# Kernel tuning notes

Hardware: AMD Instinct MI355X
Metric: run time of the kernel (lower is better)

The kernel has to match this reference:

```python
import jax, jax.numpy as jnp
import numpy as np

DEPTH = 4
NUM_INTERNAL = 2 ** DEPTH - 1  # 15
NUM_LEAVES = 2 ** DEPTH        # 16
INPUT_DIM = 1024
NUM_CLASSES = 100
LEAF_HIDDEN = 256
BATCH = 4096
TAU = 1.0
EPS = 1e-10


def setup_inputs() -> dict:
    key = jax.random.key(0)
    ks = jax.random.split(key, 8)
    x = jax.random.normal(ks[0], (BATCH, INPUT_DIM), dtype=jnp.float32)
    gumbel_u = jax.random.uniform(ks[1], (NUM_INTERNAL, BATCH, INPUT_DIM), dtype=jnp.float32)
    feature_logits = jax.random.normal(ks[2], (NUM_INTERNAL, INPUT_DIM), dtype=jnp.float32) * 0.1
    split_thresholds = jnp.zeros((NUM_INTERNAL,), dtype=jnp.float32)
    feature_weights = jax.random.normal(ks[3], (NUM_INTERNAL, INPUT_DIM), dtype=jnp.float32) / np.sqrt(INPUT_DIM)
    # leaf MLPs, kaiming-normal init (fan_in), zero bias
    W1 = jax.random.normal(ks[4], (NUM_LEAVES, LEAF_HIDDEN, INPUT_DIM), dtype=jnp.float32) * np.sqrt(2.0 / INPUT_DIM)
    b1 = jnp.zeros((NUM_LEAVES, LEAF_HIDDEN), dtype=jnp.float32)
    W2 = jax.random.normal(ks[5], (NUM_LEAVES, NUM_CLASSES, LEAF_HIDDEN), dtype=jnp.float32) * np.sqrt(2.0 / LEAF_HIDDEN)
    b2 = jnp.zeros((NUM_LEAVES, NUM_CLASSES), dtype=jnp.float32)
    return {
        'x': x, 'gumbel_u': gumbel_u,
        'feature_logits': feature_logits, 'split_thresholds': split_thresholds,
        'feature_weights': feature_weights, 'W1': W1, 'b1': b1, 'W2': W2, 'b2': b2,
    }


def reference(x, gumbel_u, feature_logits, split_thresholds, feature_weights, W1, b1, W2, b2):
    # --- Gumbel-softmax feature gating (soft, tau=TAU) for ALL nodes at once ---
    g = -jnp.log(-jnp.log(gumbel_u + EPS) + EPS)                 # [N, B, D]
    imp = jax.nn.softmax((feature_logits[:, None, :] + g) / TAU, axis=-1)  # [N, B, D]
    # aggregated split value: sum_d x * importance * feature_weight
    agg = jnp.einsum('bd,nbd,nd->nb', x, imp, feature_weights)   # [N, B]
    split_prob = jax.nn.sigmoid((agg - split_thresholds[:, None]) / TAU)   # [N, B]

    # --- leaf routing probabilities (level-order traversal) ---
    probs = jnp.ones((1, x.shape[0]), dtype=x.dtype)             # [1, B]
    for level in range(DEPTH):
        n = 2 ** level
        s = jax.lax.dynamic_slice_in_dim(split_prob, n - 1, n, axis=0)  # [n, B]
        # order per node: left then right -> interleave
        probs = jnp.stack([probs * (1.0 - s), probs * s], axis=1).reshape(2 * n, -1)
    leaf_probs = probs                                           # [L, B]

    # --- leaf MLPs (dropout is identity in eval), batched over leaves ---
    h = jax.nn.relu(jnp.einsum('bd,lhd->lbh', x, W1) + b1[:, None, :])      # [L, B, H]
    leaf_out = jnp.einsum('lbh,lch->lbc', h, W2) + b2[:, None, :]           # [L, B, C]

    # weighted combine over leaves
    logits = jnp.einsum('lbc,lb->bc', leaf_out, leaf_probs)     # [B, C]
    return logits
```

## Files before the change

kernel.cpp:

```cpp
#include <hip/hip_runtime.h>
#include <hip/hip_bf16.h>
#include <cstdint>
#include <cstddef>

#define NI 15
#define NL 16
#define DD 1024
#define NC 100
#define HH 256
#define BB 4096

typedef __attribute__((ext_vector_type(8))) short bf16x8;
typedef __attribute__((ext_vector_type(8))) unsigned short u16x8;
typedef __attribute__((ext_vector_type(4))) float f32x4;

__device__ __forceinline__ unsigned short f2bf(float f) {
  union { float f; unsigned u; } v; v.f = f;
  return (unsigned short)((v.u + 0x7FFFu + ((v.u >> 16) & 1u)) >> 16);
}

__device__ __forceinline__ void gld_lds16(const void* g, void* s) {
  __builtin_amdgcn_global_load_lds(
      (const __attribute__((address_space(1))) unsigned int*)g,
      (__attribute__((address_space(3))) unsigned int*)s, 16, 0, 0);
}

__global__ __launch_bounds__(256) void k_convert(const float* __restrict__ src,
                                                 unsigned short* __restrict__ dst,
                                                 int n) {
  const int stride = gridDim.x * blockDim.x * 4;
  for (int i = (blockIdx.x * blockDim.x + threadIdx.x) * 4; i < n; i += stride) {
    float4 v = *reinterpret_cast<const float4*>(src + i);
    ushort4 o;
    o.x = f2bf(v.x); o.y = f2bf(v.y); o.z = f2bf(v.z); o.w = f2bf(v.w);
    *reinterpret_cast<ushort4*>(dst + i) = o;
  }
}

__global__ __launch_bounds__(256) void k_gate(
    const float* __restrict__ x, const float* __restrict__ gu,
    const float* __restrict__ fl, const float* __restrict__ thr,
    const float* __restrict__ fw, float* __restrict__ split,
    unsigned short* __restrict__ xb) {
  const int b = blockIdx.x;
  const int w = threadIdx.x >> 6, lane = threadIdx.x & 63;

  float xr[16];
  const float* xp = x + (size_t)b * DD;
  for (int j = 0; j < 4; ++j) {
    float4 v = *reinterpret_cast<const float4*>(xp + lane * 4 + j * 256);
    xr[j * 4 + 0] = v.x; xr[j * 4 + 1] = v.y;
    xr[j * 4 + 2] = v.z; xr[j * 4 + 3] = v.w;
  }
  if (w == 0) {
    for (int j = 0; j < 4; ++j) {
      ushort4 o;
      o.x = f2bf(xr[j * 4 + 0]); o.y = f2bf(xr[j * 4 + 1]);
      o.z = f2bf(xr[j * 4 + 2]); o.w = f2bf(xr[j * 4 + 3]);
      *reinterpret_cast<ushort4*>(xb + (size_t)b * DD + lane * 4 + j * 256) = o;
    }
  }

  for (int n = w; n < NI; n += 4) {
    const float* gp = gu + ((size_t)n * BB + b) * DD;
    const float* fp = fl + (size_t)n * DD;
    const float* wp = fw + (size_t)n * DD;
    float num = 0.f, den = 0.f;
    for (int j = 0; j < 4; ++j) {
      const int e = lane * 4 + j * 256;
      float4 g4 = *reinterpret_cast<const float4*>(gp + e);
      float4 f4 = *reinterpret_cast<const float4*>(fp + e);
      float4 w4 = *reinterpret_cast<const float4*>(wp + e);
      float gv[4] = {g4.x, g4.y, g4.z, g4.w};
      float fv[4] = {f4.x, f4.y, f4.z, f4.w};
      float wv[4] = {w4.x, w4.y, w4.z, w4.w};
      for (int q = 0; q < 4; ++q) {
        float gg = -__logf(-__logf(gv[q] + 1e-10f) + 1e-10f);
        float e2 = __expf(fv[q] + gg);
        den += e2;
        num += xr[j * 4 + q] * wv[q] * e2;
      }
    }
    for (int off = 32; off; off >>= 1) {
      num += __shfl_xor(num, off);
      den += __shfl_xor(den, off);
    }
    if (lane == 0) {
      float agg = num / den;
      split[n * BB + b] = 1.f / (1.f + __expf(-(agg - thr[n])));
    }
  }
}

__global__ __launch_bounds__(256) void k_leaf(const float* __restrict__ split,
                                              float* __restrict__ lp) {
  const int b = blockIdx.x * blockDim.x + threadIdx.x;
  if (b >= BB) return;
  float s[NI];
  for (int i = 0; i < NI; ++i) s[i] = split[i * BB + b];
  for (int leaf = 0; leaf < NL; ++leaf) {
    float p = 1.f;
    int node = 0;
    for (int lev = 0; lev < 4; ++lev) {
      int bit = (leaf >> (3 - lev)) & 1;
      p *= bit ? s[node] : (1.f - s[node]);
      node = 2 * node + 1 + bit;
    }
    lp[(size_t)b * NL + leaf] = p;
  }
}

__global__ __launch_bounds__(256) void k_gemm1(
    const unsigned short* __restrict__ xb, const unsigned short* __restrict__ w1b,
    const float* __restrict__ b1, const float* __restrict__ lp,
    unsigned short* __restrict__ hs) {
  __shared__ unsigned short lA[128 * 64];
  __shared__ unsigned short lB[128 * 64];
  __shared__ float s_lp[128];
  __shared__ float s_b1[128];

  const int tid = threadIdx.x;
  const int mt = blockIdx.x, nt = blockIdx.y, l = blockIdx.z;
  const int m0 = mt * 128, n0 = nt * 128;

  if (tid < 128) s_lp[tid] = lp[(size_t)(m0 + tid) * NL + l];
  else           s_b1[tid - 128] = b1[l * HH + n0 + (tid - 128)];

  const unsigned short* Ag = xb + (size_t)m0 * DD;
  const unsigned short* Bg = w1b + (size_t)l * HH * DD + (size_t)n0 * DD;

  f32x4 acc[4][4] = {};
  const int wv = tid >> 6, lane = tid & 63;
  const int wm = (wv & 1) * 64, wn = (wv >> 1) * 64;
  const int fr = lane & 15, fk = (lane >> 4) * 8;
  const int srow = tid >> 3, scol = (tid & 7) * 8;

  for (int k0 = 0; k0 < DD; k0 += 64) {
    for (int i = 0; i < 4; ++i)
      gld_lds16(Ag + (size_t)(srow + i * 32) * DD + k0 + scol,
                &lA[(srow + i * 32) * 64 + scol]);
    for (int i = 0; i < 4; ++i)
      gld_lds16(Bg + (size_t)(srow + i * 32) * DD + k0 + scol,
                &lB[(srow + i * 32) * 64 + scol]);
    __syncthreads();
    for (int kk = 0; kk < 64; kk += 32) {
      bf16x8 av[4], bv[4];
      for (int i = 0; i < 4; ++i)
        av[i] = *reinterpret_cast<const bf16x8*>(&lA[(wm + i * 16 + fr) * 64 + kk + fk]);
      for (int i = 0; i < 4; ++i)
        bv[i] = *reinterpret_cast<const bf16x8*>(&lB[(wn + i * 16 + fr) * 64 + kk + fk]);
      for (int mi = 0; mi < 4; ++mi)
        for (int ni = 0; ni < 4; ++ni)
          acc[mi][ni] = __builtin_amdgcn_mfma_f32_16x16x32_bf16(av[mi], bv[ni], acc[mi][ni], 0, 0, 0);
    }
    __syncthreads();
  }

  const int cr = (lane >> 4) * 4, cc = lane & 15;
  for (int mi = 0; mi < 4; ++mi)
    for (int ni = 0; ni < 4; ++ni) {
      const int col = wn + ni * 16 + cc;
      const float bias = s_b1[col];
      for (int j = 0; j < 4; ++j) {
        const int row = wm + mi * 16 + cr + j;
        float v = acc[mi][ni][j] + bias;
        v = fmaxf(v, 0.f) * s_lp[row];
        hs[(size_t)l * BB * HH + (size_t)(m0 + row) * HH + (n0 + col)] = f2bf(v);
      }
    }
}

__global__ __launch_bounds__(256) void k_gemm2(
    const unsigned short* __restrict__ hs, const unsigned short* __restrict__ w2b,
    float* __restrict__ part) {
  __shared__ unsigned short lA[128 * 64];
  __shared__ unsigned short lB[128 * 64];

  const int tid = threadIdx.x;
  const int mt = blockIdx.x, kc = blockIdx.y;
  const int m0 = mt * 128;

  f32x4 acc[4][4] = {};
  const int wv = tid >> 6, lane = tid & 63;
  const int wm = (wv & 1) * 64, wn = (wv >> 1) * 64;
  const int fr = lane & 15, fk = (lane >> 4) * 8;
  const int srow = tid >> 3, scol = (tid & 7) * 8;

  for (int ks = 0; ks < 8; ++ks) {
    const int kg = kc * 512 + ks * 64;
    const int l = kg >> 8, h0 = kg & 255;
    const unsigned short* Ag = hs + (size_t)l * BB * HH + (size_t)m0 * HH + h0;
    for (int i = 0; i < 4; ++i)
      gld_lds16(Ag + (size_t)(srow + i * 32) * HH + scol,
                &lA[(srow + i * 32) * 64 + scol]);
    const unsigned short* Bg = w2b + (size_t)l * NC * HH + h0;
    for (int i = 0; i < 4; ++i) {
      const int c = srow + i * 32;
      u16x8 v = {};
      if (c < NC) v = *reinterpret_cast<const u16x8*>(Bg + (size_t)c * HH + scol);
      *reinterpret_cast<u16x8*>(&lB[c * 64 + scol]) = v;
    }
    __syncthreads();
    for (int kk = 0; kk < 64; kk += 32) {
      bf16x8 av[4], bv[4];
      for (int i = 0; i < 4; ++i)
        av[i] = *reinterpret_cast<const bf16x8*>(&lA[(wm + i * 16 + fr) * 64 + kk + fk]);
      for (int i = 0; i < 4; ++i)
        bv[i] = *reinterpret_cast<const bf16x8*>(&lB[(wn + i * 16 + fr) * 64 + kk + fk]);
      for (int mi = 0; mi < 4; ++mi)
        for (int ni = 0; ni < 4; ++ni)
          acc[mi][ni] = __builtin_amdgcn_mfma_f32_16x16x32_bf16(av[mi], bv[ni], acc[mi][ni], 0, 0, 0);
    }
    __syncthreads();
  }

  const int cr = (lane >> 4) * 4, cc = lane & 15;
  for (int mi = 0; mi < 4; ++mi)
    for (int ni = 0; ni < 4; ++ni) {
      const int col = wn + ni * 16 + cc;
      if (col < NC) {
        for (int j = 0; j < 4; ++j) {
          const int row = wm + mi * 16 + cr + j;
          part[((size_t)kc * BB + m0 + row) * NC + col] = acc[mi][ni][j];
        }
      }
    }
}

__global__ __launch_bounds__(256) void k_reduce(const float* __restrict__ part,
                                                const float* __restrict__ lp,
                                                const float* __restrict__ b2,
                                                float* __restrict__ out) {
  const int i = blockIdx.x * 256 + threadIdx.x;
  if (i >= BB * NC) return;
  const int b = i / NC, c = i - b * NC;
  float v = 0.f;
  for (int k = 0; k < 8; ++k) v += part[(size_t)k * BB * NC + i];
  const float* lpp = lp + (size_t)b * NL;
  for (int l = 0; l < NL; ++l) v += lpp[l] * b2[l * NC + c];
  out[i] = v;
}

extern "C" void kernel_launch(void* const* d_in, const int* in_sizes, int n_in,
                              void* d_out, int out_size, void* d_ws, size_t ws_size,
                              hipStream_t stream) {
  const float* x   = (const float*)d_in[0];
  const float* gu  = (const float*)d_in[1];
  const float* fl  = (const float*)d_in[2];
  const float* thr = (const float*)d_in[3];
  const float* fw  = (const float*)d_in[4];
  const float* W1  = (const float*)d_in[5];
  const float* b1  = (const float*)d_in[6];
  const float* W2  = (const float*)d_in[7];
  const float* b2  = (const float*)d_in[8];
  float* out = (float*)d_out;

  char* ws = (char*)d_ws;
  float* split          = (float*)(ws + 0);
  float* lp             = (float*)(ws + 245760);
  unsigned short* xb    = (unsigned short*)(ws + 507904);
  unsigned short* w1b   = (unsigned short*)(ws + 8896512);
  unsigned short* w2b   = (unsigned short*)(ws + 17285120);
  unsigned short* hsb   = (unsigned short*)(ws + 18104320);
  float* part           = (float*)(ws + 51658752);

  k_gate<<<BB, 256, 0, stream>>>(x, gu, fl, thr, fw, split, xb);
  k_convert<<<2048, 256, 0, stream>>>(W1, w1b, NL * HH * DD);
  k_convert<<<512,  256, 0, stream>>>(W2, w2b, NL * NC * HH);
  k_leaf<<<16, 256, 0, stream>>>(split, lp);

  k_gemm1<<<dim3(32, 2, 16), 256, 0, stream>>>(xb, w1b, b1, lp, hsb);
  k_gemm2<<<dim3(32, 8, 1), 256, 0, stream>>>(hsb, w2b, part);
  k_reduce<<<1600, 256, 0, stream>>>(part, lp, b2, out);
}
```

Measured before the change: 472.5 us.

## Fuse leaf routing into gate, merge weight conversion, pipeline larger gemm1 tiles

```diff
diff --git a/kernel.cpp b/kernel.cpp
--- a/kernel.cpp
+++ b/kernel.cpp
@@ -25,23 +25,30 @@
       (__attribute__((address_space(3))) unsigned int*)s, 16, 0, 0);
 }
 
-__global__ __launch_bounds__(256) void k_convert(const float* __restrict__ src,
-                                                 unsigned short* __restrict__ dst,
-                                                 int n) {
+__global__ __launch_bounds__(256) void k_convertW(const float* __restrict__ W1,
+                                                  const float* __restrict__ W2,
+                                                  unsigned short* __restrict__ w1b,
+                                                  unsigned short* __restrict__ w2b) {
+  const int n1 = NL * HH * DD;
+  const int n2 = NL * NC * HH;
   const int stride = gridDim.x * blockDim.x * 4;
-  for (int i = (blockIdx.x * blockDim.x + threadIdx.x) * 4; i < n; i += stride) {
-    float4 v = *reinterpret_cast<const float4*>(src + i);
+  for (int i = (blockIdx.x * blockDim.x + threadIdx.x) * 4; i < n1 + n2; i += stride) {
+    const float* s; unsigned short* d;
+    if (i < n1) { s = W1 + i; d = w1b + i; }
+    else        { s = W2 + (i - n1); d = w2b + (i - n1); }
+    float4 v = *reinterpret_cast<const float4*>(s);
     ushort4 o;
     o.x = f2bf(v.x); o.y = f2bf(v.y); o.z = f2bf(v.z); o.w = f2bf(v.w);
-    *reinterpret_cast<ushort4*>(dst + i) = o;
+    *reinterpret_cast<ushort4*>(d) = o;
   }
 }
 
 __global__ __launch_bounds__(256) void k_gate(
     const float* __restrict__ x, const float* __restrict__ gu,
     const float* __restrict__ fl, const float* __restrict__ thr,
-    const float* __restrict__ fw, float* __restrict__ split,
+    const float* __restrict__ fw, float* __restrict__ lp,
     unsigned short* __restrict__ xb) {
+  __shared__ float s_split[NI];
   const int b = blockIdx.x;
   const int w = threadIdx.x >> 6, lane = threadIdx.x & 63;
 
@@ -65,7 +72,7 @@
     const float* gp = gu + ((size_t)n * BB + b) * DD;
     const float* fp = fl + (size_t)n * DD;
     const float* wp = fw + (size_t)n * DD;
-    float num = 0.f, den = 0.f;
+    float num[4] = {0.f, 0.f, 0.f, 0.f}, den[4] = {0.f, 0.f, 0.f, 0.f};
     for (int j = 0; j < 4; ++j) {
       const int e = lane * 4 + j * 256;
       float4 g4 = *reinterpret_cast<const float4*>(gp + e);
@@ -77,95 +84,124 @@
       for (int q = 0; q < 4; ++q) {
         float gg = -__logf(-__logf(gv[q] + 1e-10f) + 1e-10f);
         float e2 = __expf(fv[q] + gg);
-        den += e2;
-        num += xr[j * 4 + q] * wv[q] * e2;
+        den[j] += e2;
+        num[j] += xr[j * 4 + q] * wv[q] * e2;
       }
     }
+    float nums = (num[0] + num[1]) + (num[2] + num[3]);
+    float dens = (den[0] + den[1]) + (den[2] + den[3]);
     for (int off = 32; off; off >>= 1) {
-      num += __shfl_xor(num, off);
-      den += __shfl_xor(den, off);
+      nums += __shfl_xor(nums, off);
+      dens += __shfl_xor(dens, off);
     }
     if (lane == 0) {
-      float agg = num / den;
-      split[n * BB + b] = 1.f / (1.f + __expf(-(agg - thr[n])));
-    }
-  }
-}
-
-__global__ __launch_bounds__(256) void k_leaf(const float* __restrict__ split,
-                                              float* __restrict__ lp) {
-  const int b = blockIdx.x * blockDim.x + threadIdx.x;
-  if (b >= BB) return;
-  float s[NI];
-  for (int i = 0; i < NI; ++i) s[i] = split[i * BB + b];
-  for (int leaf = 0; leaf < NL; ++leaf) {
-    float p = 1.f;
-    int node = 0;
+      float agg = nums / dens;
+      s_split[n] = 1.f / (1.f + __expf(-(agg - thr[n])));
+    }
+  }
+  __syncthreads();
+  if (threadIdx.x < NL) {
+    const int leaf = threadIdx.x;
+    float p = 1.f; int node = 0;
     for (int lev = 0; lev < 4; ++lev) {
       int bit = (leaf >> (3 - lev)) & 1;
-      p *= bit ? s[node] : (1.f - s[node]);
+      float s = s_split[node];
+      p *= bit ? s : (1.f - s);
       node = 2 * node + 1 + bit;
     }
     lp[(size_t)b * NL + leaf] = p;
   }
 }
 
-__global__ __launch_bounds__(256) void k_gemm1(
+__global__ __launch_bounds__(512, 2) void k_gemm1(
     const unsigned short* __restrict__ xb, const unsigned short* __restrict__ w1b,
     const float* __restrict__ b1, const float* __restrict__ lp,
     unsigned short* __restrict__ hs) {
-  __shared__ unsigned short lA[128 * 64];
-  __shared__ unsigned short lB[128 * 64];
-  __shared__ float s_lp[128];
-  __shared__ float s_b1[128];
+  __shared__ unsigned short lA[3][256 * 32];
+  __shared__ unsigned short lB[3][256 * 32];
+  __shared__ float s_lp[256];
+  __shared__ float s_b1[256];
 
   const int tid = threadIdx.x;
-  const int mt = blockIdx.x, nt = blockIdx.y, l = blockIdx.z;
-  const int m0 = mt * 128, n0 = nt * 128;
-
-  if (tid < 128) s_lp[tid] = lp[(size_t)(m0 + tid) * NL + l];
-  else           s_b1[tid - 128] = b1[l * HH + n0 + (tid - 128)];
-
-  const unsigned short* Ag = xb + (size_t)m0 * DD;
-  const unsigned short* Bg = w1b + (size_t)l * HH * DD + (size_t)n0 * DD;
-
-  f32x4 acc[4][4] = {};
-  const int wv = tid >> 6, lane = tid & 63;
-  const int wm = (wv & 1) * 64, wn = (wv >> 1) * 64;
-  const int fr = lane & 15, fk = (lane >> 4) * 8;
-  const int srow = tid >> 3, scol = (tid & 7) * 8;
-
-  for (int k0 = 0; k0 < DD; k0 += 64) {
-    for (int i = 0; i < 4; ++i)
-      gld_lds16(Ag + (size_t)(srow + i * 32) * DD + k0 + scol,
-                &lA[(srow + i * 32) * 64 + scol]);
-    for (int i = 0; i < 4; ++i)
-      gld_lds16(Bg + (size_t)(srow + i * 32) * DD + k0 + scol,
-                &lB[(srow + i * 32) * 64 + scol]);
-    __syncthreads();
-    for (int kk = 0; kk < 64; kk += 32) {
-      bf16x8 av[4], bv[4];
-      for (int i = 0; i < 4; ++i)
-        av[i] = *reinterpret_cast<const bf16x8*>(&lA[(wm + i * 16 + fr) * 64 + kk + fk]);
-      for (int i = 0; i < 4; ++i)
-        bv[i] = *reinterpret_cast<const bf16x8*>(&lB[(wn + i * 16 + fr) * 64 + kk + fk]);
-      for (int mi = 0; mi < 4; ++mi)
-        for (int ni = 0; ni < 4; ++ni)
-          acc[mi][ni] = __builtin_amdgcn_mfma_f32_16x16x32_bf16(av[mi], bv[ni], acc[mi][ni], 0, 0, 0);
-    }
-    __syncthreads();
-  }
+  const int l = blockIdx.x, mt = blockIdx.y;
+  const int m0 = mt * 256;
+
+  if (tid < 256) s_lp[tid] = lp[(size_t)(m0 + tid) * NL + l];
+  else           s_b1[tid & 255] = b1[l * HH + (tid & 255)];
+
+  const unsigned short* Ag = xb  + (size_t)m0 * DD;
+  const unsigned short* Bg = w1b + (size_t)l * HH * DD;
+
+  const int srow = tid >> 2;
+  const int scol = (tid & 3) * 8;
+
+  __syncthreads();
+
+#define STAGE1(tt, bb) do {                                                       \
+    const int kk_ = (tt) * 32;                                                    \
+    gld_lds16(Ag + (size_t)srow * DD + kk_ + scol,         &lA[bb][srow * 32 + scol]);         \
+    gld_lds16(Ag + (size_t)(srow + 128) * DD + kk_ + scol, &lA[bb][(srow + 128) * 32 + scol]); \
+    gld_lds16(Bg + (size_t)srow * DD + kk_ + scol,         &lB[bb][srow * 32 + scol]);         \
+    gld_lds16(Bg + (size_t)(srow + 128) * DD + kk_ + scol, &lB[bb][(srow + 128) * 32 + scol]); \
+  } while (0)
+
+  STAGE1(0, 0); STAGE1(1, 1); STAGE1(2, 2);
+
+  const int wid = tid >> 6, lane = tid & 63;
+  const int wr = wid >> 2, wc = wid & 3;
+  const int g8 = (lane >> 4) * 8, fr = lane & 15;
+
+  f32x4 acc[8][4] = {};
+
+  int bufi = 0;
+  for (int t = 0; t < 32; ++t) {
+    const int rem = 31 - t;
+    if (rem >= 2)      { asm volatile("s_waitcnt vmcnt(8)" ::: "memory"); }
+    else if (rem == 1) { asm volatile("s_waitcnt vmcnt(4)" ::: "memory"); }
+    else               { asm volatile("s_waitcnt vmcnt(0)" ::: "memory"); }
+    __builtin_amdgcn_s_barrier();
+    __builtin_amdgcn_sched_barrier(0);
+
+    const unsigned short* bA = lA[bufi];
+    const unsigned short* bB = lB[bufi];
+    bf16x8 av[8], bv[4];
+#pragma unroll
+    for (int mi = 0; mi < 8; ++mi)
+      av[mi] = *reinterpret_cast<const bf16x8*>(&bA[(wr * 128 + mi * 16 + fr) * 32 + g8]);
+#pragma unroll
+    for (int nj = 0; nj < 4; ++nj)
+      bv[nj] = *reinterpret_cast<const bf16x8*>(&bB[(wc * 64 + nj * 16 + fr) * 32 + g8]);
+
+    __builtin_amdgcn_s_setprio(1);
+#pragma unroll
+    for (int mi = 0; mi < 8; ++mi)
+#pragma unroll
+      for (int nj = 0; nj < 4; ++nj)
+        acc[mi][nj] = __builtin_amdgcn_mfma_f32_16x16x32_bf16(av[mi], bv[nj], acc[mi][nj], 0, 0, 0);
+    __builtin_amdgcn_s_setprio(0);
+
+    __builtin_amdgcn_sched_barrier(0);
+    __builtin_amdgcn_s_barrier();
+    __builtin_amdgcn_sched_barrier(0);
+    if (t + 3 < 32) STAGE1(t + 3, bufi);
+    bufi = (bufi == 2) ? 0 : bufi + 1;
+  }
+#undef STAGE1
 
   const int cr = (lane >> 4) * 4, cc = lane & 15;
-  for (int mi = 0; mi < 4; ++mi)
-    for (int ni = 0; ni < 4; ++ni) {
-      const int col = wn + ni * 16 + cc;
+  unsigned short* Hp = hs + (size_t)l * BB * HH;
+#pragma unroll
+  for (int mi = 0; mi < 8; ++mi)
+#pragma unroll
+    for (int nj = 0; nj < 4; ++nj) {
+      const int col = wc * 64 + nj * 16 + cc;
       const float bias = s_b1[col];
+#pragma unroll
       for (int j = 0; j < 4; ++j) {
-        const int row = wm + mi * 16 + cr + j;
-        float v = acc[mi][ni][j] + bias;
+        const int row = wr * 128 + mi * 16 + cr + j;
+        float v = acc[mi][nj][j] + bias;
         v = fmaxf(v, 0.f) * s_lp[row];
-        hs[(size_t)l * BB * HH + (size_t)(m0 + row) * HH + (n0 + col)] = f2bf(v);
+        Hp[(size_t)(m0 + row) * HH + col] = f2bf(v);
       }
     }
 }
@@ -256,20 +292,17 @@
   float* out = (float*)d_out;
 
   char* ws = (char*)d_ws;
-  float* split          = (float*)(ws + 0);
-  float* lp             = (float*)(ws + 245760);
-  unsigned short* xb    = (unsigned short*)(ws + 507904);
-  unsigned short* w1b   = (unsigned short*)(ws + 8896512);
-  unsigned short* w2b   = (unsigned short*)(ws + 17285120);
-  unsigned short* hsb   = (unsigned short*)(ws + 18104320);
-  float* part           = (float*)(ws + 51658752);
-
-  k_gate<<<BB, 256, 0, stream>>>(x, gu, fl, thr, fw, split, xb);
-  k_convert<<<2048, 256, 0, stream>>>(W1, w1b, NL * HH * DD);
-  k_convert<<<512,  256, 0, stream>>>(W2, w2b, NL * NC * HH);
-  k_leaf<<<16, 256, 0, stream>>>(split, lp);
-
-  k_gemm1<<<dim3(32, 2, 16), 256, 0, stream>>>(xb, w1b, b1, lp, hsb);
-  k_gemm2<<<dim3(32, 8, 1), 256, 0, stream>>>(hsb, w2b, part);
+  float* lp             = (float*)(ws + 0);
+  unsigned short* xb    = (unsigned short*)(ws + 262144);
+  unsigned short* w1b   = (unsigned short*)(ws + 8650752);
+  unsigned short* w2b   = (unsigned short*)(ws + 17039360);
+  unsigned short* hsb   = (unsigned short*)(ws + 17858560);
+  float* part           = (float*)(ws + 51412992);
+
+  k_gate<<<BB, 256, 0, stream>>>(x, gu, fl, thr, fw, lp, xb);
+  k_convertW<<<2048, 256, 0, stream>>>(W1, W2, w1b, w2b);
+
+  k_gemm1<<<dim3(16, 16), 512, 0, stream>>>(xb, w1b, b1, lp, hsb);
+  k_gemm2<<<dim3(32, 8), 256, 0, stream>>>(hsb, w2b, part);
   k_reduce<<<1600, 256, 0, stream>>>(part, lp, b2, out);
 }
```

Result: faster. 459.1 us (-2.8%).
